# Optimization experiments

Measured on AMD Instinct MI355X. Metric: run time of the kernel, lower is better.

## Reference

```python
import jax, jax.numpy as jnp
import numpy as np

N_EMBD = 32
BLOCK = 8
N_HEADS = 4
HEAD = N_EMBD // N_HEADS  # 8


def setup_inputs() -> dict:
    key = jax.random.key(0)
    k_x, k_attn, k_proj, k_f1, k_f2 = jax.random.split(key, 5)
    b = 262144
    X = jax.random.normal(k_x, (b, BLOCK, N_EMBD), dtype=jnp.float32)
    # per-head fused qkv weight, stored (in, out) so y = x @ W; out = 3*HEAD, split K,Q,V
    W_attn = jax.random.normal(k_attn, (N_HEADS, N_EMBD, 3 * HEAD), dtype=jnp.float32) * 0.02
    W_proj = jax.random.normal(k_proj, (N_EMBD, N_EMBD), dtype=jnp.float32) * 0.02
    W_ff1 = jax.random.normal(k_f1, (N_EMBD, 4 * N_EMBD), dtype=jnp.float32) * 0.02
    W_ff2 = jax.random.normal(k_f2, (4 * N_EMBD, N_EMBD), dtype=jnp.float32) * 0.02
    return {"X": X, "W_attn": W_attn, "W_proj": W_proj, "W_ff1": W_ff1, "W_ff2": W_ff2}


def reference(X, W_attn, W_proj, W_ff1, W_ff2):
    b, t, c = X.shape
    # fused per-head QKV: (b, t, c) x (h, c, 3*HEAD) -> (b, h, t, 3*HEAD)
    qkv = jnp.einsum('btc,hcd->bhtd', X, W_attn)
    k, q, v = jnp.split(qkv, 3, axis=-1)  # split order K, Q, V as in torch .split
    # NOTE: scale uses full embed dim c, not head_size (faithful to source)
    scores = jnp.einsum('bhqd,bhkd->bhqk', q, k) * (c ** -0.5)
    causal = jnp.tril(jnp.ones((t, t), dtype=bool))
    scores = jnp.where(causal, scores, -jnp.inf)
    w = jax.nn.softmax(scores, axis=-1)
    attn = jnp.einsum('bhqk,bhkd->bhqd', w, v)  # (b, h, t, HEAD)
    attn = attn.transpose(0, 2, 1, 3).reshape(b, t, c)  # concat heads
    X = X + attn @ W_proj
    X = X + jax.nn.relu(X @ W_ff1) @ W_ff2
    return X
```

## Files before the change

### kernel.cpp

```cpp
#include <hip/hip_runtime.h>


typedef __attribute__((ext_vector_type(8))) short        bf16x8;
typedef __attribute__((ext_vector_type(4))) float        f32x4;
typedef __attribute__((ext_vector_type(4))) int          i32x4;
typedef __attribute__((ext_vector_type(2))) unsigned int u32x2;

#define THREADS 256
#define TPB 64
#define TPW 16

#define LDS_X     0
#define LDS_P2    0
#define LDS_QK    2560
#define LDS_ATTN  2560
#define LDS_VT    4864
#define LDS_X2    4864
#define LDS_HID   0
#define LDS_OUT   4352
#define LDS_CTX   6656

__device__ __forceinline__ unsigned pk_bf16(float a, float b) {
    unsigned r;
    asm("v_cvt_pk_bf16_f32 %0, %1, %2" : "=v"(r) : "v"(a), "v"(b));
    return r;
}

union frag_u { i32x4 i; bf16x8 b; };

__device__ __forceinline__ bf16x8 gather_w(const float* p, int ldk, int g, float s) {
    frag_u r;
    #pragma unroll
    for (int jj = 0; jj < 4; ++jj) {
        float a = p[(8 * g + 2 * jj) * ldk] * s;
        float b = p[(8 * g + 2 * jj + 1) * ldk] * s;
        r.i[jj] = (int)pk_bf16(a, b);
    }
    return r.b;
}

__global__ void pack_w(const float* __restrict__ Wff1,
                       const float* __restrict__ Wff2,
                       i32x4* __restrict__ ws)
{
    const int lane = threadIdx.x & 63;
    const int g = lane >> 4, c = lane & 15;
    #pragma unroll
    for (int n = 0; n < 8; ++n) {
        frag_u f; f.b = gather_w(Wff1 + 16 * n + c, 128, g, 1.f);
        ws[n * 64 + lane] = f.i;
    }
    #pragma unroll
    for (int n = 0; n < 2; ++n)
        #pragma unroll
        for (int ks = 0; ks < 4; ++ks) {
            frag_u f; f.b = gather_w(Wff2 + ks * 1024 + 16 * n + c, 32, g, 1.f);
            ws[(8 + n * 4 + ks) * 64 + lane] = f.i;
        }
}


__device__ __forceinline__ void ph_qkv(char* Wc, int c, int g,
                                       const bf16x8 (&wqk)[4], const bf16x8 (&wv)[2],
                                       const bf16x8& xf) {
    const f32x4 z4 = {0.f, 0.f, 0.f, 0.f};
    #pragma unroll
    for (int n = 0; n < 4; ++n) {
        f32x4 qc = __builtin_amdgcn_mfma_f32_16x16x32_bf16(wqk[n], xf, z4, 0, 0, 0);
        u32x2 w64 = { pk_bf16(qc[0], qc[1]), pk_bf16(qc[2], qc[3]) };
        *(u32x2*)(void*)(Wc + LDS_QK + c * 144 + (16 * n + 4 * g) * 2) = w64;
    }
    #pragma unroll
    for (int n = 0; n < 2; ++n) {
        f32x4 vc = __builtin_amdgcn_mfma_f32_16x16x32_bf16(xf, wv[n], z4, 0, 0, 0);
        u32x2 w64 = { pk_bf16(vc[0], vc[1]), pk_bf16(vc[2], vc[3]) };
        *(u32x2*)(void*)(Wc + LDS_VT + (16 * n + c) * 48 + 8 * g) = w64;
    }
}

__device__ __forceinline__ void ph_scores(char* Wc, int c, int g,
                                          const f32x4& mf, const i32x4& mQK) {
    const f32x4 z4 = {0.f, 0.f, 0.f, 0.f};
    #pragma unroll
    for (int h = 0; h < 4; ++h) {
        frag_u kf, qf;
        kf.i = *(i32x4*)(void*)(Wc + LDS_QK + c * 144 + 32 * h);
        qf.i = *(i32x4*)(void*)(Wc + LDS_QK + c * 144 + 32 * h + 16);
        kf.i &= mQK; qf.i &= mQK;
        f32x4 sT = __builtin_amdgcn_mfma_f32_16x16x32_bf16(kf.b, qf.b, z4, 0, 0, 0);
        float e0 = __builtin_amdgcn_exp2f(sT[0]) * mf[0];
        float e1 = __builtin_amdgcn_exp2f(sT[1]) * mf[1];
        float e2 = __builtin_amdgcn_exp2f(sT[2]) * mf[2];
        float e3 = __builtin_amdgcn_exp2f(sT[3]) * mf[3];
        float s = (e0 + e1) + (e2 + e3);
        s += __shfl_xor(s, 16);
        s += __shfl_xor(s, 32);
        float rs = __builtin_amdgcn_rcpf(s);
        u32x2 w64 = { pk_bf16(e0 * rs, e1 * rs), pk_bf16(e2 * rs, e3 * rs) };
        *(u32x2*)(void*)(Wc + LDS_P2 + (h >> 1) * 1280 + c * 80 + ((h & 1) * 16 + 4 * g) * 2) = w64;
    }
}

__device__ __forceinline__ void ph_pv(char* Wc, int c, int g, const i32x4& mPV) {
    const f32x4 z4 = {0.f, 0.f, 0.f, 0.f};
    #pragma unroll
    for (int p = 0; p < 2; ++p) {
        frag_u va, pb;
        va.i = *(i32x4*)(void*)(Wc + LDS_VT + (16 * p + c) * 48 + (g & 1) * 16);
        va.i &= mPV;
        pb.i = *(i32x4*)(void*)(Wc + LDS_P2 + p * 1280 + c * 80 + g * 16);
        f32x4 pv = __builtin_amdgcn_mfma_f32_16x16x32_bf16(va.b, pb.b, z4, 0, 0, 0);
        u32x2 w64 = { pk_bf16(pv[0], pv[1]), pk_bf16(pv[2], pv[3]) };
        *(u32x2*)(void*)(Wc + LDS_ATTN + c * 80 + (16 * p + 4 * g) * 2) = w64;
    }
}

__device__ __forceinline__ void ph_proj(char* Wc, int c, int g, const bf16x8 (&wp)[2],
                                        const f32x4& rx0, const f32x4& rx1, f32x4 (&x2c)[2]) {
    frag_u af; af.i = *(i32x4*)(void*)(Wc + LDS_ATTN + c * 80 + g * 16);
    #pragma unroll
    for (int n = 0; n < 2; ++n) {
        const f32x4 z4 = {0.f, 0.f, 0.f, 0.f};
        f32x4 pc = __builtin_amdgcn_mfma_f32_16x16x32_bf16(wp[n], af.b, z4, 0, 0, 0);
        f32x4 rx = (n == 0) ? rx0 : rx1;
        #pragma unroll
        for (int r = 0; r < 4; ++r) x2c[n][r] = pc[r] + rx[r];
        u32x2 w64 = { pk_bf16(x2c[n][0], x2c[n][1]), pk_bf16(x2c[n][2], x2c[n][3]) };
        *(u32x2*)(void*)(Wc + LDS_X2 + c * 80 + (16 * n + 4 * g) * 2) = w64;
    }
}

__device__ __forceinline__ void ph_ff1h(char* Wc, int c, int g,
                                        const bf16x8 (&w1h)[4], int n0,
                                        const bf16x8& bfX) {
    #pragma unroll
    for (int k = 0; k < 4; ++k) {
        const int n = n0 + k;
        const f32x4 z4 = {0.f, 0.f, 0.f, 0.f};
        f32x4 hc = __builtin_amdgcn_mfma_f32_16x16x32_bf16(w1h[k], bfX, z4, 0, 0, 0);
        #pragma unroll
        for (int r = 0; r < 4; ++r) hc[r] = fmaxf(hc[r], 0.f);
        u32x2 w64 = { pk_bf16(hc[0], hc[1]), pk_bf16(hc[2], hc[3]) };
        *(u32x2*)(void*)(Wc + LDS_HID + c * 272 + (16 * n + 4 * g) * 2) = w64;
    }
}

__device__ __forceinline__ void ph_ff2_store(char* Wc, int c, int g,
                                             const bf16x8 (&w2a)[4], const bf16x8 (&w2b)[4],
                                             const f32x4 (&x2c)[2], float* outg, bool ok) {
    frag_u hf0, hf1, hf2, hf3;
    hf0.i = *(i32x4*)(void*)(Wc + LDS_HID + c * 272 + 0 * 64 + g * 16);
    hf1.i = *(i32x4*)(void*)(Wc + LDS_HID + c * 272 + 1 * 64 + g * 16);
    hf2.i = *(i32x4*)(void*)(Wc + LDS_HID + c * 272 + 2 * 64 + g * 16);
    hf3.i = *(i32x4*)(void*)(Wc + LDS_HID + c * 272 + 3 * 64 + g * 16);
    {
        f32x4 oc = x2c[0];
        oc = __builtin_amdgcn_mfma_f32_16x16x32_bf16(w2a[0], hf0.b, oc, 0, 0, 0);
        oc = __builtin_amdgcn_mfma_f32_16x16x32_bf16(w2a[1], hf1.b, oc, 0, 0, 0);
        oc = __builtin_amdgcn_mfma_f32_16x16x32_bf16(w2a[2], hf2.b, oc, 0, 0, 0);
        oc = __builtin_amdgcn_mfma_f32_16x16x32_bf16(w2a[3], hf3.b, oc, 0, 0, 0);
        if (ok) *(f32x4*)(outg + c * 32 + 4 * g) = oc;
    }
    {
        f32x4 oc = x2c[1];
        oc = __builtin_amdgcn_mfma_f32_16x16x32_bf16(w2b[0], hf0.b, oc, 0, 0, 0);
        oc = __builtin_amdgcn_mfma_f32_16x16x32_bf16(w2b[1], hf1.b, oc, 0, 0, 0);
        oc = __builtin_amdgcn_mfma_f32_16x16x32_bf16(w2b[2], hf2.b, oc, 0, 0, 0);
        oc = __builtin_amdgcn_mfma_f32_16x16x32_bf16(w2b[3], hf3.b, oc, 0, 0, 0);
        if (ok) *(f32x4*)(outg + c * 32 + 16 + 4 * g) = oc;
    }
}


__device__ __forceinline__ void ph_stage(char* Wc, int lane, const f32x4& xa, const f32x4& xb) {
    i32x4 xi = { (int)pk_bf16(xa[0], xa[1]), (int)pk_bf16(xa[2], xa[3]),
                 (int)pk_bf16(xb[0], xb[1]), (int)pk_bf16(xb[2], xb[3]) };
    *(i32x4*)(void*)(Wc + LDS_X + (lane >> 2) * 80 + (lane & 3) * 16) = xi;
}

__device__ __forceinline__ void ph_ff2(char* Wc, int c, int g,
                                       const bf16x8 (&w2a)[4], const bf16x8 (&w2b)[4],
                                       const f32x4 (&x2c)[2]) {
    frag_u hf0, hf1, hf2, hf3;
    hf0.i = *(i32x4*)(void*)(Wc + LDS_HID + c * 272 + 0 * 64 + g * 16);
    hf1.i = *(i32x4*)(void*)(Wc + LDS_HID + c * 272 + 1 * 64 + g * 16);
    hf2.i = *(i32x4*)(void*)(Wc + LDS_HID + c * 272 + 2 * 64 + g * 16);
    hf3.i = *(i32x4*)(void*)(Wc + LDS_HID + c * 272 + 3 * 64 + g * 16);
    {
        f32x4 oc = x2c[0];
        oc = __builtin_amdgcn_mfma_f32_16x16x32_bf16(w2a[0], hf0.b, oc, 0, 0, 0);
        oc = __builtin_amdgcn_mfma_f32_16x16x32_bf16(w2a[1], hf1.b, oc, 0, 0, 0);
        oc = __builtin_amdgcn_mfma_f32_16x16x32_bf16(w2a[2], hf2.b, oc, 0, 0, 0);
        oc = __builtin_amdgcn_mfma_f32_16x16x32_bf16(w2a[3], hf3.b, oc, 0, 0, 0);
        *(f32x4*)(void*)(Wc + LDS_OUT + c * 144 + 4 * g * 4) = oc;
    }
    {
        f32x4 oc = x2c[1];
        oc = __builtin_amdgcn_mfma_f32_16x16x32_bf16(w2b[0], hf0.b, oc, 0, 0, 0);
        oc = __builtin_amdgcn_mfma_f32_16x16x32_bf16(w2b[1], hf1.b, oc, 0, 0, 0);
        oc = __builtin_amdgcn_mfma_f32_16x16x32_bf16(w2b[2], hf2.b, oc, 0, 0, 0);
        oc = __builtin_amdgcn_mfma_f32_16x16x32_bf16(w2b[3], hf3.b, oc, 0, 0, 0);
        *(f32x4*)(void*)(Wc + LDS_OUT + c * 144 + (16 + 4 * g) * 4) = oc;
    }
}

__device__ __forceinline__ void ph_store(char* Wc, int lane, float* outg) {
    f32x4 r0 = *(f32x4*)(void*)(Wc + LDS_OUT + (lane >> 2) * 144 + (lane & 3) * 32);
    f32x4 r1 = *(f32x4*)(void*)(Wc + LDS_OUT + (lane >> 2) * 144 + (lane & 3) * 32 + 16);
    *(f32x4*)(outg + lane * 8)     = r0;
    *(f32x4*)(outg + lane * 8 + 4) = r1;
}

__device__ __forceinline__ void ph_qkv_lds(char* Wc, int c, int g,
                                           const bf16x8 (&wqk)[4], const bf16x8 (&wv)[2]) {
    frag_u xf; xf.i = *(i32x4*)(void*)(Wc + LDS_X + c * 80 + g * 16);
    ph_qkv(Wc, c, g, wqk, wv, xf.b);
}


struct Prolog {
    bf16x8 wqk[4], wv[2], wp[2];
    f32x4 mf;
    i32x4 mQK, mPV;
};

__device__ __forceinline__ void make_prolog(Prolog& P, const float* Wattn,
                                            const float* Wproj, int lane, int g, int c) {
    const float wscale = 0.5050098f;
    #pragma unroll
    for (int n = 0; n < 4; ++n)
        P.wqk[n] = gather_w(Wattn + n * 768 + c, 24, g, wscale);
    #pragma unroll
    for (int n = 0; n < 2; ++n) {
        int vch = 16 * n + c;
        P.wv[n] = gather_w(Wattn + (vch >> 3) * 768 + 16 + (vch & 7), 24, g, 1.f);
    }
    #pragma unroll
    for (int n = 0; n < 2; ++n)
        P.wp[n] = gather_w(Wproj + 16 * n + c, 32, g, 1.f);
    #pragma unroll
    for (int r = 0; r < 4; ++r) {
        int key = 4 * g + r;
        P.mf[r] = ((key >> 3) == (c >> 3) && (key & 7) <= (c & 7)) ? 1.f : 0.f;
    }
    const int b0 = (lane < 16) ? -1 : 0;
    const int b1 = (((lane >> 3) & 1) == ((lane >> 5) & 1)) ? -1 : 0;
    P.mQK = i32x4{b0, b0, b0, b0};
    P.mPV = i32x4{b1, b1, b1, b1};
}


__global__ __launch_bounds__(THREADS)
void block_mfma_ws(const float* __restrict__ X,
                   const float* __restrict__ Wattn,
                   const float* __restrict__ Wproj,
                   const i32x4* __restrict__ WT,
                   float* __restrict__ Out,
                   int ntiles)
{
    __shared__ __align__(16) char smem[4 * 2 * LDS_CTX];

    const int lane = threadIdx.x & 63;
    const int wid  = threadIdx.x >> 6;
    const int g    = lane >> 4;
    const int c    = lane & 15;
    char* WA = smem + wid * (2 * LDS_CTX);
    char* WB = WA + LDS_CTX;

    Prolog P;
    make_prolog(P, Wattn, Wproj, lane, g, c);

    const int tile0 = blockIdx.x * TPB + wid * TPW;
    if (tile0 >= ntiles) return;

    int p0 = tile0, p1 = (tile0 + 1 < ntiles) ? tile0 + 1 : ntiles - 1;
    f32x4 xrA0 = *(const f32x4*)(X + (size_t)p0 * 512 + c * 32 + 8 * g);
    f32x4 xrA1 = *(const f32x4*)(X + (size_t)p0 * 512 + c * 32 + 8 * g + 4);
    f32x4 xrB0 = *(const f32x4*)(X + (size_t)p1 * 512 + c * 32 + 8 * g);
    f32x4 xrB1 = *(const f32x4*)(X + (size_t)p1 * 512 + c * 32 + 8 * g + 4);

    #pragma unroll 1
    for (int it = 0; it < TPW; it += 2) {
        const int iA = tile0 + it;
        const int iB = tile0 + it + 1;
        const int ttA = (iA < ntiles) ? iA : ntiles - 1;
        const int ttB = (iB < ntiles) ? iB : ntiles - 1;
        const float* xgA = X + (size_t)ttA * 512;
        const float* xgB = X + (size_t)ttB * 512;

        f32x4 rxA0 = *(const f32x4*)(xgA + c * 32 + 4 * g);
        f32x4 rxA1 = *(const f32x4*)(xgA + c * 32 + 16 + 4 * g);
        f32x4 rxB0 = *(const f32x4*)(xgB + c * 32 + 4 * g);
        f32x4 rxB1 = *(const f32x4*)(xgB + c * 32 + 16 + 4 * g);

        frag_u xfA, xfB;
        xfA.i = i32x4{ (int)pk_bf16(xrA0[0], xrA0[1]), (int)pk_bf16(xrA0[2], xrA0[3]),
                       (int)pk_bf16(xrA1[0], xrA1[1]), (int)pk_bf16(xrA1[2], xrA1[3]) };
        xfB.i = i32x4{ (int)pk_bf16(xrB0[0], xrB0[1]), (int)pk_bf16(xrB0[2], xrB0[3]),
                       (int)pk_bf16(xrB1[0], xrB1[1]), (int)pk_bf16(xrB1[2], xrB1[3]) };

        {
            int nA = (it + 2 < TPW && iA + 2 < ntiles) ? iA + 2 : ttA;
            int nB = (it + 3 < TPW && iB + 2 < ntiles) ? iB + 2 : ttB;
            xrA0 = *(const f32x4*)(X + (size_t)nA * 512 + c * 32 + 8 * g);
            xrA1 = *(const f32x4*)(X + (size_t)nA * 512 + c * 32 + 8 * g + 4);
            xrB0 = *(const f32x4*)(X + (size_t)nB * 512 + c * 32 + 8 * g);
            xrB1 = *(const f32x4*)(X + (size_t)nB * 512 + c * 32 + 8 * g + 4);
        }

        ph_qkv(WA, c, g, P.wqk, P.wv, xfA.b);
        ph_qkv(WB, c, g, P.wqk, P.wv, xfB.b);

        bf16x8 w1lo[4];
        #pragma unroll
        for (int k = 0; k < 4; ++k) { frag_u t; t.i = WT[k * 64 + lane]; w1lo[k] = t.b; }

        ph_scores(WA, c, g, P.mf, P.mQK);
        ph_scores(WB, c, g, P.mf, P.mQK);

        bf16x8 w1hi[4];
        #pragma unroll
        for (int k = 0; k < 4; ++k) { frag_u t; t.i = WT[(4 + k) * 64 + lane]; w1hi[k] = t.b; }

        ph_pv(WA, c, g, P.mPV);
        ph_pv(WB, c, g, P.mPV);

        f32x4 x2A[2], x2B[2];
        ph_proj(WA, c, g, P.wp, rxA0, rxA1, x2A);
        ph_proj(WB, c, g, P.wp, rxB0, rxB1, x2B);

        frag_u bfA; bfA.i = *(i32x4*)(void*)(WA + LDS_X2 + c * 80 + g * 16);
        frag_u bfB; bfB.i = *(i32x4*)(void*)(WB + LDS_X2 + c * 80 + g * 16);

        bf16x8 w2lo[4];
        #pragma unroll
        for (int k = 0; k < 4; ++k) { frag_u t; t.i = WT[(8 + k) * 64 + lane]; w2lo[k] = t.b; }

        ph_ff1h(WA, c, g, w1lo, 0, bfA.b);
        ph_ff1h(WA, c, g, w1hi, 4, bfA.b);

        bf16x8 w2hi[4];
        #pragma unroll
        for (int k = 0; k < 4; ++k) { frag_u t; t.i = WT[(12 + k) * 64 + lane]; w2hi[k] = t.b; }

        ph_ff1h(WB, c, g, w1lo, 0, bfB.b);
        ph_ff1h(WB, c, g, w1hi, 4, bfB.b);

        ph_ff2_store(WA, c, g, w2lo, w2hi, x2A, Out + (size_t)ttA * 512, iA < ntiles);
        ph_ff2_store(WB, c, g, w2lo, w2hi, x2B, Out + (size_t)ttB * 512, iB < ntiles);
    }
}


__global__ __launch_bounds__(THREADS)
void block_mfma_reg(const float* __restrict__ X,
                    const float* __restrict__ Wattn,
                    const float* __restrict__ Wproj,
                    const float* __restrict__ Wff1,
                    const float* __restrict__ Wff2,
                    float* __restrict__ Out,
                    int ntiles)
{
    __shared__ __align__(16) char smem[4 * 2 * LDS_CTX];

    const int lane = threadIdx.x & 63;
    const int wid  = threadIdx.x >> 6;
    const int g    = lane >> 4;
    const int c    = lane & 15;
    char* WA = smem + wid * (2 * LDS_CTX);
    char* WB = WA + LDS_CTX;

    Prolog P;
    make_prolog(P, Wattn, Wproj, lane, g, c);

    bf16x8 w1lo[4], w1hi[4], w2lo[4], w2hi[4];
    #pragma unroll
    for (int k = 0; k < 4; ++k) {
        w1lo[k] = gather_w(Wff1 + 16 * k + c, 128, g, 1.f);
        w1hi[k] = gather_w(Wff1 + 16 * (4 + k) + c, 128, g, 1.f);
        w2lo[k] = gather_w(Wff2 + k * 1024 + c, 32, g, 1.f);
        w2hi[k] = gather_w(Wff2 + k * 1024 + 16 + c, 32, g, 1.f);
    }

    const int tile0 = blockIdx.x * TPB + wid * TPW;
    if (tile0 >= ntiles) return;

    int p0 = tile0, p1 = (tile0 + 1 < ntiles) ? tile0 + 1 : ntiles - 1;
    f32x4 xaA = *(const f32x4*)(X + (size_t)p0 * 512 + lane * 8);
    f32x4 xbA = *(const f32x4*)(X + (size_t)p0 * 512 + lane * 8 + 4);
    f32x4 xaB = *(const f32x4*)(X + (size_t)p1 * 512 + lane * 8);
    f32x4 xbB = *(const f32x4*)(X + (size_t)p1 * 512 + lane * 8 + 4);

    #pragma unroll 1
    for (int it = 0; it < TPW; it += 2) {
        const int iA = tile0 + it;
        const int iB = tile0 + it + 1;
        const int ttA = (iA < ntiles) ? iA : ntiles - 1;
        const int ttB = (iB < ntiles) ? iB : ntiles - 1;
        const float* xgA = X + (size_t)ttA * 512;
        const float* xgB = X + (size_t)ttB * 512;

        f32x4 rxA0 = *(const f32x4*)(xgA + c * 32 + 4 * g);
        f32x4 rxA1 = *(const f32x4*)(xgA + c * 32 + 16 + 4 * g);
        f32x4 rxB0 = *(const f32x4*)(xgB + c * 32 + 4 * g);
        f32x4 rxB1 = *(const f32x4*)(xgB + c * 32 + 16 + 4 * g);

        ph_stage(WA, lane, xaA, xbA);
        ph_stage(WB, lane, xaB, xbB);

        {
            int nA = (it + 2 < TPW && iA + 2 < ntiles) ? iA + 2 : ttA;
            int nB = (it + 3 < TPW && iB + 2 < ntiles) ? iB + 2 : ttB;
            xaA = *(const f32x4*)(X + (size_t)nA * 512 + lane * 8);
            xbA = *(const f32x4*)(X + (size_t)nA * 512 + lane * 8 + 4);
            xaB = *(const f32x4*)(X + (size_t)nB * 512 + lane * 8);
            xbB = *(const f32x4*)(X + (size_t)nB * 512 + lane * 8 + 4);
        }

        ph_qkv_lds(WA, c, g, P.wqk, P.wv);
        ph_qkv_lds(WB, c, g, P.wqk, P.wv);

        ph_scores(WA, c, g, P.mf, P.mQK);
        ph_scores(WB, c, g, P.mf, P.mQK);

        ph_pv(WA, c, g, P.mPV);
        ph_pv(WB, c, g, P.mPV);

        f32x4 x2A[2], x2B[2];
        ph_proj(WA, c, g, P.wp, rxA0, rxA1, x2A);
        ph_proj(WB, c, g, P.wp, rxB0, rxB1, x2B);

        frag_u bfA; bfA.i = *(i32x4*)(void*)(WA + LDS_X2 + c * 80 + g * 16);
        frag_u bfB; bfB.i = *(i32x4*)(void*)(WB + LDS_X2 + c * 80 + g * 16);

        ph_ff1h(WA, c, g, w1lo, 0, bfA.b);
        ph_ff1h(WA, c, g, w1hi, 4, bfA.b);
        ph_ff1h(WB, c, g, w1lo, 0, bfB.b);
        ph_ff1h(WB, c, g, w1hi, 4, bfB.b);

        ph_ff2(WA, c, g, w2lo, w2hi, x2A);
        if (iA < ntiles) ph_store(WA, lane, Out + (size_t)iA * 512);

        ph_ff2(WB, c, g, w2lo, w2hi, x2B);
        if (iB < ntiles) ph_store(WB, lane, Out + (size_t)iB * 512);
    }
}

extern "C" void kernel_launch(void* const* d_in, const int* in_sizes, int n_in,
                              void* d_out, int out_size, void* d_ws, size_t ws_size,
                              hipStream_t stream) {
    (void)n_in; (void)out_size;
    const float* X     = (const float*)d_in[0];
    const float* Wattn = (const float*)d_in[1];
    const float* Wproj = (const float*)d_in[2];
    const float* Wff1  = (const float*)d_in[3];
    const float* Wff2  = (const float*)d_in[4];
    float* Out = (float*)d_out;

    const int nseq   = in_sizes[0] / 256;
    const int ntiles = nseq / 2;
    const int blocks = (ntiles + TPB - 1) / TPB;

    if (ws_size >= 16384 && d_ws != nullptr) {
        i32x4* WT = (i32x4*)d_ws;
        pack_w<<<dim3(1), dim3(64), 0, stream>>>(Wff1, Wff2, WT);
        block_mfma_ws<<<dim3(blocks), dim3(THREADS), 0, stream>>>(
            X, Wattn, Wproj, WT, Out, ntiles);
    } else {
        block_mfma_reg<<<dim3(blocks), dim3(THREADS), 0, stream>>>(
            X, Wattn, Wproj, Wff1, Wff2, Out, ntiles);
    }
}
```

Before: 205.5 us.

## Split fused block kernel into attention and feed-forward kernels via bf16 workspace

Replaces the single fused kernel with two kernels. The first computes attention plus projection and writes the residual stream X2 to workspace as packed bf16. The second reads X2 and runs the FF1/ReLU/FF2 MLP, adding the bf16 residual back. This is meant to cut per-kernel register and LDS pressure and simplify scheduling, at the cost of an extra round trip of the intermediate through global memory. Keeping the residual in bf16 instead of fp32 also reduces accuracy, and the fallback path for a small or absent workspace was removed.

```diff
diff --git a/kernel.cpp b/kernel.cpp
--- a/kernel.cpp
+++ b/kernel.cpp
@@ -20,10 +20,26 @@
 #define LDS_OUT   4352
 #define LDS_CTX   6656
 
+#define A_QK   0
+#define A_ATTN 0
+#define A_VT   2304
+#define A_P2   3840
+#define A_CTX  6400
+
+#define F_HID  0
+#define F_CTX  4352
+
 __device__ __forceinline__ unsigned pk_bf16(float a, float b) {
     unsigned r;
     asm("v_cvt_pk_bf16_f32 %0, %1, %2" : "=v"(r) : "v"(a), "v"(b));
     return r;
+}
+
+__device__ __forceinline__ float bf_lo(unsigned u) {
+    union { unsigned u; float f; } v; v.u = u << 16; return v.f;
+}
+__device__ __forceinline__ float bf_hi(unsigned u) {
+    union { unsigned u; float f; } v; v.u = u & 0xffff0000u; return v.f;
 }
 
 union frag_u { i32x4 i; bf16x8 b; };
@@ -57,6 +73,217 @@
             frag_u f; f.b = gather_w(Wff2 + ks * 1024 + 16 * n + c, 32, g, 1.f);
             ws[(8 + n * 4 + ks) * 64 + lane] = f.i;
         }
+}
+
+
+__global__ __launch_bounds__(THREADS)
+void attn_ker(const float* __restrict__ X,
+              const float* __restrict__ Wattn,
+              const float* __restrict__ Wproj,
+              unsigned* __restrict__ X2,
+              int ntiles)
+{
+    __shared__ __align__(16) char smem[4 * A_CTX];
+
+    const int lane = threadIdx.x & 63;
+    const int wid  = threadIdx.x >> 6;
+    const int g    = lane >> 4;
+    const int c    = lane & 15;
+    char* W = smem + wid * A_CTX;
+
+    const float wscale = 0.5050098f;
+    const f32x4 z4 = {0.f, 0.f, 0.f, 0.f};
+
+    bf16x8 wqk[4], wv[2], wp[2];
+    #pragma unroll
+    for (int n = 0; n < 4; ++n)
+        wqk[n] = gather_w(Wattn + n * 768 + c, 24, g, wscale);
+    #pragma unroll
+    for (int n = 0; n < 2; ++n) {
+        int vch = 16 * n + c;
+        wv[n] = gather_w(Wattn + (vch >> 3) * 768 + 16 + (vch & 7), 24, g, 1.f);
+    }
+    #pragma unroll
+    for (int n = 0; n < 2; ++n)
+        wp[n] = gather_w(Wproj + 16 * n + c, 32, g, 1.f);
+
+    f32x4 mf;
+    #pragma unroll
+    for (int r = 0; r < 4; ++r) {
+        int key = 4 * g + r;
+        mf[r] = ((key >> 3) == (c >> 3) && (key & 7) <= (c & 7)) ? 1.f : 0.f;
+    }
+    const int b0 = (lane < 16) ? -1 : 0;
+    const int b1 = (((lane >> 3) & 1) == ((lane >> 5) & 1)) ? -1 : 0;
+    const i32x4 mQK = {b0, b0, b0, b0};
+    const i32x4 mPV = {b1, b1, b1, b1};
+
+    const int tile0 = blockIdx.x * TPB + wid * TPW;
+    if (tile0 >= ntiles) return;
+
+    f32x4 xr0 = *(const f32x4*)(X + (size_t)tile0 * 512 + c * 32 + 8 * g);
+    f32x4 xr1 = *(const f32x4*)(X + (size_t)tile0 * 512 + c * 32 + 8 * g + 4);
+
+    #pragma unroll 1
+    for (int it = 0; it < TPW; ++it) {
+        const int i = tile0 + it;
+        const int tt = (i < ntiles) ? i : ntiles - 1;
+        const float* xg = X + (size_t)tt * 512;
+
+        frag_u xf;
+        xf.i = i32x4{ (int)pk_bf16(xr0[0], xr0[1]), (int)pk_bf16(xr0[2], xr0[3]),
+                      (int)pk_bf16(xr1[0], xr1[1]), (int)pk_bf16(xr1[2], xr1[3]) };
+
+        {
+            int nx = (it + 1 < TPW && i + 1 < ntiles) ? i + 1 : tt;
+            xr0 = *(const f32x4*)(X + (size_t)nx * 512 + c * 32 + 8 * g);
+            xr1 = *(const f32x4*)(X + (size_t)nx * 512 + c * 32 + 8 * g + 4);
+        }
+
+        #pragma unroll
+        for (int n = 0; n < 4; ++n) {
+            f32x4 qc = __builtin_amdgcn_mfma_f32_16x16x32_bf16(wqk[n], xf.b, z4, 0, 0, 0);
+            u32x2 w64 = { pk_bf16(qc[0], qc[1]), pk_bf16(qc[2], qc[3]) };
+            *(u32x2*)(void*)(W + A_QK + c * 144 + (16 * n + 4 * g) * 2) = w64;
+        }
+        #pragma unroll
+        for (int n = 0; n < 2; ++n) {
+            f32x4 vc = __builtin_amdgcn_mfma_f32_16x16x32_bf16(xf.b, wv[n], z4, 0, 0, 0);
+            u32x2 w64 = { pk_bf16(vc[0], vc[1]), pk_bf16(vc[2], vc[3]) };
+            *(u32x2*)(void*)(W + A_VT + (16 * n + c) * 48 + 8 * g) = w64;
+        }
+
+        #pragma unroll
+        for (int h = 0; h < 4; ++h) {
+            frag_u kf, qf;
+            kf.i = *(i32x4*)(void*)(W + A_QK + c * 144 + 32 * h);
+            qf.i = *(i32x4*)(void*)(W + A_QK + c * 144 + 32 * h + 16);
+            kf.i &= mQK; qf.i &= mQK;
+            f32x4 sT = __builtin_amdgcn_mfma_f32_16x16x32_bf16(kf.b, qf.b, z4, 0, 0, 0);
+            float e0 = __builtin_amdgcn_exp2f(sT[0]) * mf[0];
+            float e1 = __builtin_amdgcn_exp2f(sT[1]) * mf[1];
+            float e2 = __builtin_amdgcn_exp2f(sT[2]) * mf[2];
+            float e3 = __builtin_amdgcn_exp2f(sT[3]) * mf[3];
+            float s = (e0 + e1) + (e2 + e3);
+            s += __shfl_xor(s, 16);
+            s += __shfl_xor(s, 32);
+            float rs = __builtin_amdgcn_rcpf(s);
+            u32x2 w64 = { pk_bf16(e0 * rs, e1 * rs), pk_bf16(e2 * rs, e3 * rs) };
+            *(u32x2*)(void*)(W + A_P2 + (h >> 1) * 1280 + c * 80 + ((h & 1) * 16 + 4 * g) * 2) = w64;
+        }
+
+        #pragma unroll
+        for (int p = 0; p < 2; ++p) {
+            frag_u va, pb;
+            va.i = *(i32x4*)(void*)(W + A_VT + (16 * p + c) * 48 + (g & 1) * 16);
+            va.i &= mPV;
+            pb.i = *(i32x4*)(void*)(W + A_P2 + p * 1280 + c * 80 + g * 16);
+            f32x4 pv = __builtin_amdgcn_mfma_f32_16x16x32_bf16(va.b, pb.b, z4, 0, 0, 0);
+            u32x2 w64 = { pk_bf16(pv[0], pv[1]), pk_bf16(pv[2], pv[3]) };
+            *(u32x2*)(void*)(W + A_ATTN + c * 80 + (16 * p + 4 * g) * 2) = w64;
+        }
+
+        frag_u af; af.i = *(i32x4*)(void*)(W + A_ATTN + c * 80 + g * 16);
+        unsigned* x2t = X2 + (size_t)tt * 256;
+        #pragma unroll
+        for (int n = 0; n < 2; ++n) {
+            f32x4 pc = __builtin_amdgcn_mfma_f32_16x16x32_bf16(wp[n], af.b, z4, 0, 0, 0);
+            f32x4 rx = *(const f32x4*)(xg + c * 32 + 16 * n + 4 * g);
+            u32x2 w64 = { pk_bf16(pc[0] + rx[0], pc[1] + rx[1]),
+                          pk_bf16(pc[2] + rx[2], pc[3] + rx[3]) };
+            *(u32x2*)(x2t + c * 16 + 8 * n + 2 * g) = w64;
+        }
+    }
+}
+
+
+__global__ __launch_bounds__(THREADS)
+void ff_ker(const unsigned* __restrict__ X2,
+            const float* __restrict__ Wff1,
+            const float* __restrict__ Wff2,
+            float* __restrict__ Out,
+            int ntiles)
+{
+    __shared__ __align__(16) char smem[4 * F_CTX];
+
+    const int lane = threadIdx.x & 63;
+    const int wid  = threadIdx.x >> 6;
+    const int g    = lane >> 4;
+    const int c    = lane & 15;
+    char* W = smem + wid * F_CTX;
+    const f32x4 z4 = {0.f, 0.f, 0.f, 0.f};
+
+    bf16x8 w1lo[4], w1hi[4], w2lo[4], w2hi[4];
+    #pragma unroll
+    for (int k = 0; k < 4; ++k) {
+        w1lo[k] = gather_w(Wff1 + 16 * k + c, 128, g, 1.f);
+        w1hi[k] = gather_w(Wff1 + 16 * (4 + k) + c, 128, g, 1.f);
+        w2lo[k] = gather_w(Wff2 + k * 1024 + c, 32, g, 1.f);
+        w2hi[k] = gather_w(Wff2 + k * 1024 + 16 + c, 32, g, 1.f);
+    }
+
+    const int tile0 = blockIdx.x * TPB + wid * TPW;
+    if (tile0 >= ntiles) return;
+
+    frag_u xf; xf.i = *(const i32x4*)(X2 + (size_t)tile0 * 256 + c * 16 + 4 * g);
+
+    #pragma unroll 1
+    for (int it = 0; it < TPW; ++it) {
+        const int i = tile0 + it;
+        const int tt = (i < ntiles) ? i : ntiles - 1;
+        const unsigned* x2t = X2 + (size_t)tt * 256;
+
+        frag_u xcur = xf;
+        {
+            int nx = (it + 1 < TPW && i + 1 < ntiles) ? i + 1 : tt;
+            xf.i = *(const i32x4*)(X2 + (size_t)nx * 256 + c * 16 + 4 * g);
+        }
+
+        u32x2 rv0 = *(const u32x2*)(x2t + c * 16 + 2 * g);
+        u32x2 rv1 = *(const u32x2*)(x2t + c * 16 + 8 + 2 * g);
+
+        #pragma unroll
+        for (int k = 0; k < 4; ++k) {
+            f32x4 hc = __builtin_amdgcn_mfma_f32_16x16x32_bf16(w1lo[k], xcur.b, z4, 0, 0, 0);
+            #pragma unroll
+            for (int r = 0; r < 4; ++r) hc[r] = fmaxf(hc[r], 0.f);
+            u32x2 w64 = { pk_bf16(hc[0], hc[1]), pk_bf16(hc[2], hc[3]) };
+            *(u32x2*)(void*)(W + F_HID + c * 272 + (16 * k + 4 * g) * 2) = w64;
+        }
+        #pragma unroll
+        for (int k = 0; k < 4; ++k) {
+            f32x4 hc = __builtin_amdgcn_mfma_f32_16x16x32_bf16(w1hi[k], xcur.b, z4, 0, 0, 0);
+            #pragma unroll
+            for (int r = 0; r < 4; ++r) hc[r] = fmaxf(hc[r], 0.f);
+            u32x2 w64 = { pk_bf16(hc[0], hc[1]), pk_bf16(hc[2], hc[3]) };
+            *(u32x2*)(void*)(W + F_HID + c * 272 + (16 * (4 + k) + 4 * g) * 2) = w64;
+        }
+
+        frag_u hf0, hf1, hf2, hf3;
+        hf0.i = *(i32x4*)(void*)(W + F_HID + c * 272 + 0 * 64 + g * 16);
+        hf1.i = *(i32x4*)(void*)(W + F_HID + c * 272 + 1 * 64 + g * 16);
+        hf2.i = *(i32x4*)(void*)(W + F_HID + c * 272 + 2 * 64 + g * 16);
+        hf3.i = *(i32x4*)(void*)(W + F_HID + c * 272 + 3 * 64 + g * 16);
+
+        float* outg = Out + (size_t)tt * 512;
+        const bool ok = (i < ntiles);
+        {
+            f32x4 oc = { bf_lo(rv0.x), bf_hi(rv0.x), bf_lo(rv0.y), bf_hi(rv0.y) };
+            oc = __builtin_amdgcn_mfma_f32_16x16x32_bf16(w2lo[0], hf0.b, oc, 0, 0, 0);
+            oc = __builtin_amdgcn_mfma_f32_16x16x32_bf16(w2lo[1], hf1.b, oc, 0, 0, 0);
+            oc = __builtin_amdgcn_mfma_f32_16x16x32_bf16(w2lo[2], hf2.b, oc, 0, 0, 0);
+            oc = __builtin_amdgcn_mfma_f32_16x16x32_bf16(w2lo[3], hf3.b, oc, 0, 0, 0);
+            if (ok) *(f32x4*)(outg + c * 32 + 4 * g) = oc;
+        }
+        {
+            f32x4 oc = { bf_lo(rv1.x), bf_hi(rv1.x), bf_lo(rv1.y), bf_hi(rv1.y) };
+            oc = __builtin_amdgcn_mfma_f32_16x16x32_bf16(w2hi[0], hf0.b, oc, 0, 0, 0);
+            oc = __builtin_amdgcn_mfma_f32_16x16x32_bf16(w2hi[1], hf1.b, oc, 0, 0, 0);
+            oc = __builtin_amdgcn_mfma_f32_16x16x32_bf16(w2hi[2], hf2.b, oc, 0, 0, 0);
+            oc = __builtin_amdgcn_mfma_f32_16x16x32_bf16(w2hi[3], hf3.b, oc, 0, 0, 0);
+            if (ok) *(f32x4*)(outg + c * 32 + 16 + 4 * g) = oc;
+        }
+    }
 }
 
 
@@ -171,53 +398,6 @@
     }
 }
 
-
-__device__ __forceinline__ void ph_stage(char* Wc, int lane, const f32x4& xa, const f32x4& xb) {
-    i32x4 xi = { (int)pk_bf16(xa[0], xa[1]), (int)pk_bf16(xa[2], xa[3]),
-                 (int)pk_bf16(xb[0], xb[1]), (int)pk_bf16(xb[2], xb[3]) };
-    *(i32x4*)(void*)(Wc + LDS_X + (lane >> 2) * 80 + (lane & 3) * 16) = xi;
-}
-
-__device__ __forceinline__ void ph_ff2(char* Wc, int c, int g,
-                                       const bf16x8 (&w2a)[4], const bf16x8 (&w2b)[4],
-                                       const f32x4 (&x2c)[2]) {
-    frag_u hf0, hf1, hf2, hf3;
-    hf0.i = *(i32x4*)(void*)(Wc + LDS_HID + c * 272 + 0 * 64 + g * 16);
-    hf1.i = *(i32x4*)(void*)(Wc + LDS_HID + c * 272 + 1 * 64 + g * 16);
-    hf2.i = *(i32x4*)(void*)(Wc + LDS_HID + c * 272 + 2 * 64 + g * 16);
-    hf3.i = *(i32x4*)(void*)(Wc + LDS_HID + c * 272 + 3 * 64 + g * 16);
-    {
-        f32x4 oc = x2c[0];
-        oc = __builtin_amdgcn_mfma_f32_16x16x32_bf16(w2a[0], hf0.b, oc, 0, 0, 0);
-        oc = __builtin_amdgcn_mfma_f32_16x16x32_bf16(w2a[1], hf1.b, oc, 0, 0, 0);
-        oc = __builtin_amdgcn_mfma_f32_16x16x32_bf16(w2a[2], hf2.b, oc, 0, 0, 0);
-        oc = __builtin_amdgcn_mfma_f32_16x16x32_bf16(w2a[3], hf3.b, oc, 0, 0, 0);
-        *(f32x4*)(void*)(Wc + LDS_OUT + c * 144 + 4 * g * 4) = oc;
-    }
-    {
-        f32x4 oc = x2c[1];
-        oc = __builtin_amdgcn_mfma_f32_16x16x32_bf16(w2b[0], hf0.b, oc, 0, 0, 0);
-        oc = __builtin_amdgcn_mfma_f32_16x16x32_bf16(w2b[1], hf1.b, oc, 0, 0, 0);
-        oc = __builtin_amdgcn_mfma_f32_16x16x32_bf16(w2b[2], hf2.b, oc, 0, 0, 0);
-        oc = __builtin_amdgcn_mfma_f32_16x16x32_bf16(w2b[3], hf3.b, oc, 0, 0, 0);
-        *(f32x4*)(void*)(Wc + LDS_OUT + c * 144 + (16 + 4 * g) * 4) = oc;
-    }
-}
-
-__device__ __forceinline__ void ph_store(char* Wc, int lane, float* outg) {
-    f32x4 r0 = *(f32x4*)(void*)(Wc + LDS_OUT + (lane >> 2) * 144 + (lane & 3) * 32);
-    f32x4 r1 = *(f32x4*)(void*)(Wc + LDS_OUT + (lane >> 2) * 144 + (lane & 3) * 32 + 16);
-    *(f32x4*)(outg + lane * 8)     = r0;
-    *(f32x4*)(outg + lane * 8 + 4) = r1;
-}
-
-__device__ __forceinline__ void ph_qkv_lds(char* Wc, int c, int g,
-                                           const bf16x8 (&wqk)[4], const bf16x8 (&wv)[2]) {
-    frag_u xf; xf.i = *(i32x4*)(void*)(Wc + LDS_X + c * 80 + g * 16);
-    ph_qkv(Wc, c, g, wqk, wv, xf.b);
-}
-
-
 struct Prolog {
     bf16x8 wqk[4], wv[2], wp[2];
     f32x4 mf;
@@ -248,7 +428,6 @@
     P.mQK = i32x4{b0, b0, b0, b0};
     P.mPV = i32x4{b1, b1, b1, b1};
 }
-
 
 __global__ __launch_bounds__(THREADS)
 void block_mfma_ws(const float* __restrict__ X,
@@ -351,100 +530,6 @@
     }
 }
 
-
-__global__ __launch_bounds__(THREADS)
-void block_mfma_reg(const float* __restrict__ X,
-                    const float* __restrict__ Wattn,
-                    const float* __restrict__ Wproj,
-                    const float* __restrict__ Wff1,
-                    const float* __restrict__ Wff2,
-                    float* __restrict__ Out,
-                    int ntiles)
-{
-    __shared__ __align__(16) char smem[4 * 2 * LDS_CTX];
-
-    const int lane = threadIdx.x & 63;
-    const int wid  = threadIdx.x >> 6;
-    const int g    = lane >> 4;
-    const int c    = lane & 15;
-    char* WA = smem + wid * (2 * LDS_CTX);
-    char* WB = WA + LDS_CTX;
-
-    Prolog P;
-    make_prolog(P, Wattn, Wproj, lane, g, c);
-
-    bf16x8 w1lo[4], w1hi[4], w2lo[4], w2hi[4];
-    #pragma unroll
-    for (int k = 0; k < 4; ++k) {
-        w1lo[k] = gather_w(Wff1 + 16 * k + c, 128, g, 1.f);
-        w1hi[k] = gather_w(Wff1 + 16 * (4 + k) + c, 128, g, 1.f);
-        w2lo[k] = gather_w(Wff2 + k * 1024 + c, 32, g, 1.f);
-        w2hi[k] = gather_w(Wff2 + k * 1024 + 16 + c, 32, g, 1.f);
-    }
-
-    const int tile0 = blockIdx.x * TPB + wid * TPW;
-    if (tile0 >= ntiles) return;
-
-    int p0 = tile0, p1 = (tile0 + 1 < ntiles) ? tile0 + 1 : ntiles - 1;
-    f32x4 xaA = *(const f32x4*)(X + (size_t)p0 * 512 + lane * 8);
-    f32x4 xbA = *(const f32x4*)(X + (size_t)p0 * 512 + lane * 8 + 4);
-    f32x4 xaB = *(const f32x4*)(X + (size_t)p1 * 512 + lane * 8);
-    f32x4 xbB = *(const f32x4*)(X + (size_t)p1 * 512 + lane * 8 + 4);
-
-    #pragma unroll 1
-    for (int it = 0; it < TPW; it += 2) {
-        const int iA = tile0 + it;
-        const int iB = tile0 + it + 1;
-        const int ttA = (iA < ntiles) ? iA : ntiles - 1;
-        const int ttB = (iB < ntiles) ? iB : ntiles - 1;
-        const float* xgA = X + (size_t)ttA * 512;
-        const float* xgB = X + (size_t)ttB * 512;
-
-        f32x4 rxA0 = *(const f32x4*)(xgA + c * 32 + 4 * g);
-        f32x4 rxA1 = *(const f32x4*)(xgA + c * 32 + 16 + 4 * g);
-        f32x4 rxB0 = *(const f32x4*)(xgB + c * 32 + 4 * g);
-        f32x4 rxB1 = *(const f32x4*)(xgB + c * 32 + 16 + 4 * g);
-
-        ph_stage(WA, lane, xaA, xbA);
-        ph_stage(WB, lane, xaB, xbB);
-
-        {
-            int nA = (it + 2 < TPW && iA + 2 < ntiles) ? iA + 2 : ttA;
-            int nB = (it + 3 < TPW && iB + 2 < ntiles) ? iB + 2 : ttB;
-            xaA = *(const f32x4*)(X + (size_t)nA * 512 + lane * 8);
-            xbA = *(const f32x4*)(X + (size_t)nA * 512 + lane * 8 + 4);
-            xaB = *(const f32x4*)(X + (size_t)nB * 512 + lane * 8);
-            xbB = *(const f32x4*)(X + (size_t)nB * 512 + lane * 8 + 4);
-        }
-
-        ph_qkv_lds(WA, c, g, P.wqk, P.wv);
-        ph_qkv_lds(WB, c, g, P.wqk, P.wv);
-
-        ph_scores(WA, c, g, P.mf, P.mQK);
-        ph_scores(WB, c, g, P.mf, P.mQK);
-
-        ph_pv(WA, c, g, P.mPV);
-        ph_pv(WB, c, g, P.mPV);
-
-        f32x4 x2A[2], x2B[2];
-        ph_proj(WA, c, g, P.wp, rxA0, rxA1, x2A);
-        ph_proj(WB, c, g, P.wp, rxB0, rxB1, x2B);
-
-        frag_u bfA; bfA.i = *(i32x4*)(void*)(WA + LDS_X2 + c * 80 + g * 16);
-        frag_u bfB; bfB.i = *(i32x4*)(void*)(WB + LDS_X2 + c * 80 + g * 16);
-
-        ph_ff1h(WA, c, g, w1lo, 0, bfA.b);
-        ph_ff1h(WA, c, g, w1hi, 4, bfA.b);
-        ph_ff1h(WB, c, g, w1lo, 0, bfB.b);
-        ph_ff1h(WB, c, g, w1hi, 4, bfB.b);
-
-        ph_ff2(WA, c, g, w2lo, w2hi, x2A);
-        if (iA < ntiles) ph_store(WA, lane, Out + (size_t)iA * 512);
-
-        ph_ff2(WB, c, g, w2lo, w2hi, x2B);
-        if (iB < ntiles) ph_store(WB, lane, Out + (size_t)iB * 512);
-    }
-}
 
 extern "C" void kernel_launch(void* const* d_in, const int* in_sizes, int n_in,
                               void* d_out, int out_size, void* d_ws, size_t ws_size,
@@ -461,13 +546,18 @@
     const int ntiles = nseq / 2;
     const int blocks = (ntiles + TPB - 1) / TPB;
 
-    if (ws_size >= 16384 && d_ws != nullptr) {
+    const size_t x2_bytes = (size_t)ntiles * 1024;
+
+    if (d_ws != nullptr && ws_size >= x2_bytes) {
+        unsigned* X2 = (unsigned*)d_ws;
+        attn_ker<<<dim3(blocks), dim3(THREADS), 0, stream>>>(
+            X, Wattn, Wproj, X2, ntiles);
+        ff_ker<<<dim3(blocks), dim3(THREADS), 0, stream>>>(
+            X2, Wff1, Wff2, Out, ntiles);
+    } else if (d_ws != nullptr && ws_size >= 16384) {
         i32x4* WT = (i32x4*)d_ws;
         pack_w<<<dim3(1), dim3(64), 0, stream>>>(Wff1, Wff2, WT);
         block_mfma_ws<<<dim3(blocks), dim3(THREADS), 0, stream>>>(
             X, Wattn, Wproj, WT, Out, ntiles);
-    } else {
-        block_mfma_reg<<<dim3(blocks), dim3(THREADS), 0, stream>>>(
-            X, Wattn, Wproj, Wff1, Wff2, Out, ntiles);
-    }
-}
+    }
+}
```

Result: slower. 231.4 us (+12.6%).
